# Kernel tuning notes

Measured on AMD Instinct MI355X. Metric: run time of the kernel, lower is better.

The kernel has to match this reference:

```python
import jax, jax.numpy as jnp
import numpy as np
from jax import lax

EPS = 1e-06


def setup_inputs() -> dict:
    key = jax.random.key(0)
    # mel-spectrogram energies: non-negative, shape (batch, n_mels, time)
    E = jax.random.uniform(key, (32, 256, 4096), dtype=jnp.float32)
    s = jnp.array([0.025], dtype=jnp.float32)
    alpha = jnp.array([0.98], dtype=jnp.float32)
    delta = jnp.array([2.0], dtype=jnp.float32)
    r = jnp.array([0.25], dtype=jnp.float32)
    return {"E": E, "s": s, "alpha": alpha, "delta": delta, "r": r}


def _iir(E, s):
    # first-order EMA over the last (time) axis: M[t] = (1-s)*M[t-1] + s*E[t], M[0] = E[0]
    s_c = jnp.clip(s, 0.0, 1.0)[0]  # scalar
    xT = jnp.moveaxis(E, -1, 0)  # (T, B, F) time-major for scan

    def step(m, x):
        m = (1.0 - s_c) * m + s_c * x
        return m, m

    _, MT = lax.scan(step, xT[0], xT[1:])
    M = jnp.concatenate([xT[:1], MT], axis=0)  # (T, B, F)
    return jnp.moveaxis(M, 0, -1)  # (B, F, T)


def reference(E, s, alpha, delta, r):
    # NOTE: original torch code computes clamped alpha/r but then uses the
    # raw self.alpha / self.r in the PCEN formula; we reproduce that exactly.
    M = _iir(E, s)
    pcen = (E / (EPS + M) ** alpha + delta) ** r - delta ** r
    pmin = pcen.min()
    pmax = pcen.max()
    return 2.0 * (pcen - pmin) / (pmax - pmin) - 1.0
```

## Files before the change

kernel.cpp:

```cpp
#include <hip/hip_runtime.h>

static constexpr int T_LEN = 4096;
static constexpr int GROUPS = T_LEN / 256;
#define EPSV 1e-6f

typedef float vfloat4 __attribute__((ext_vector_type(4)));

__device__ __forceinline__ float fexp2(float x) { return __builtin_amdgcn_exp2f(x); }
__device__ __forceinline__ float flog2(float x) { return __builtin_amdgcn_logf(x); }

__device__ __forceinline__ unsigned int flip_f(float f) {
    unsigned int u = __float_as_uint(f);
    return u ^ ((u >> 31) ? 0xFFFFFFFFu : 0x80000000u);
}
__device__ __forceinline__ float unflip_f(unsigned int u) {
    u ^= ((u >> 31) ? 0x80000000u : 0xFFFFFFFFu);
    return __uint_as_float(u);
}

__global__ void init_ws(unsigned int* ws) {
    ws[0] = 0xFFFFFFFFu;
    ws[1] = 0x00000000u;
}

template <int PASS>
__launch_bounds__(256, 4)
__global__ void pcen_pass(const float* __restrict__ E,
                          const float* __restrict__ sp,
                          const float* __restrict__ ap,
                          const float* __restrict__ dp,
                          const float* __restrict__ rp,
                          float* __restrict__ out,
                          unsigned int* __restrict__ ws,
                          int rows)
{
    const int tid  = threadIdx.x;
    const int lane = tid & 63;
    const int wv   = tid >> 6;
    const int row  = blockIdx.x * 4 + wv;

    float s = sp[0];
    s = fminf(fmaxf(s, 0.0f), 1.0f);
    const float a     = 1.0f - s;
    const float alpha = ap[0];
    const float delta = dp[0];
    const float r     = rp[0];
    const float na    = -alpha;
    const float dr    = fexp2(r * flog2(delta));

    const float a2 = a * a, a4 = a2 * a2, a8 = a4 * a4, a16 = a8 * a8,
                a32 = a16 * a16, a64 = a32 * a32, a128 = a64 * a64,
                a256 = a128 * a128;
    float pwl;
    if (a > 0.0f) pwl = fexp2((float)(4 * lane) * flog2(a));
    else          pwl = (lane == 0) ? 1.0f : 0.0f;

    float scale = 0.0f, bias = 0.0f;
    if (PASS == 1) {
        const float pmin = unflip_f(ws[0]);
        const float pmax = unflip_f(ws[1]);
        const float inv  = 2.0f / (pmax - pmin);
        scale = inv;
        bias  = __builtin_fmaf(-pmin, inv, -1.0f);
    }

    float vmin = __builtin_inff(), vmax = -__builtin_inff();

    if (row < rows) {
        const float4* __restrict__ src = (const float4*)(E + (size_t)row * T_LEN);
        float* __restrict__ drow = out + (size_t)row * T_LEN;

        float carry = E[(size_t)row * T_LEN];
        float4 cur = src[lane];

        for (int g = 0; g < GROUPS; ++g) {
            float4 nxt = make_float4(0.f, 0.f, 0.f, 0.f);
            if (g + 1 < GROUPS) nxt = src[(g + 1) * 64 + lane];

            float b = cur.x;
            b = __builtin_fmaf(a, b, cur.y);
            b = __builtin_fmaf(a, b, cur.z);
            b = __builtin_fmaf(a, b, cur.w);
            float B = s * b;

            float t;
            t = __shfl_up(B, 1, 64);  if (lane >= 1)  B = __builtin_fmaf(a4,   t, B);
            t = __shfl_up(B, 2, 64);  if (lane >= 2)  B = __builtin_fmaf(a8,   t, B);
            t = __shfl_up(B, 4, 64);  if (lane >= 4)  B = __builtin_fmaf(a16,  t, B);
            t = __shfl_up(B, 8, 64);  if (lane >= 8)  B = __builtin_fmaf(a32,  t, B);
            t = __shfl_up(B, 16, 64); if (lane >= 16) B = __builtin_fmaf(a64,  t, B);
            t = __shfl_up(B, 32, 64); if (lane >= 32) B = __builtin_fmaf(a128, t, B);

            float Bex = __shfl_up(B, 1, 64);
            if (lane == 0) Bex = 0.0f;
            const float B63 = __shfl(B, 63, 64);

            float m = __builtin_fmaf(pwl, carry, Bex);
            carry   = __builtin_fmaf(a256, carry, B63);

            float4 o;
            float p;
            m = __builtin_fmaf(a, m, s * cur.x);
            p = fexp2(r * flog2(__builtin_fmaf(cur.x, fexp2(na * flog2(EPSV + m)), delta))) - dr;
            if (PASS == 0) { vmin = fminf(vmin, p); vmax = fmaxf(vmax, p); }
            else            o.x = __builtin_fmaf(p, scale, bias);

            m = __builtin_fmaf(a, m, s * cur.y);
            p = fexp2(r * flog2(__builtin_fmaf(cur.y, fexp2(na * flog2(EPSV + m)), delta))) - dr;
            if (PASS == 0) { vmin = fminf(vmin, p); vmax = fmaxf(vmax, p); }
            else            o.y = __builtin_fmaf(p, scale, bias);

            m = __builtin_fmaf(a, m, s * cur.z);
            p = fexp2(r * flog2(__builtin_fmaf(cur.z, fexp2(na * flog2(EPSV + m)), delta))) - dr;
            if (PASS == 0) { vmin = fminf(vmin, p); vmax = fmaxf(vmax, p); }
            else            o.z = __builtin_fmaf(p, scale, bias);

            m = __builtin_fmaf(a, m, s * cur.w);
            p = fexp2(r * flog2(__builtin_fmaf(cur.w, fexp2(na * flog2(EPSV + m)), delta))) - dr;
            if (PASS == 0) { vmin = fminf(vmin, p); vmax = fmaxf(vmax, p); }
            else            o.w = __builtin_fmaf(p, scale, bias);

            if (PASS == 1) {
                vfloat4 ov = { o.x, o.y, o.z, o.w };
                __builtin_nontemporal_store(ov, (vfloat4*)(drow + (size_t)(g * 64 + lane) * 4));
            }
            cur = nxt;
        }
    }

    if (PASS == 0) {
        for (int off = 32; off >= 1; off >>= 1) {
            vmin = fminf(vmin, __shfl_xor(vmin, off, 64));
            vmax = fmaxf(vmax, __shfl_xor(vmax, off, 64));
        }
        __shared__ unsigned int smin, smax;
        if (tid == 0) { smin = 0xFFFFFFFFu; smax = 0u; }
        __syncthreads();
        if (lane == 0 && row < rows) {
            atomicMin(&smin, flip_f(vmin));
            atomicMax(&smax, flip_f(vmax));
        }
        __syncthreads();
        if (tid == 0) {
            atomicMin(&ws[0], smin);
            atomicMax(&ws[1], smax);
        }
    }
}

extern "C" void kernel_launch(void* const* d_in, const int* in_sizes, int n_in,
                              void* d_out, int out_size, void* d_ws, size_t ws_size,
                              hipStream_t stream) {
    const float* E     = (const float*)d_in[0];
    const float* s     = (const float*)d_in[1];
    const float* alpha = (const float*)d_in[2];
    const float* delta = (const float*)d_in[3];
    const float* r     = (const float*)d_in[4];
    float* out         = (float*)d_out;
    unsigned int* ws   = (unsigned int*)d_ws;

    const int rows   = in_sizes[0] / T_LEN;
    const int blocks = (rows + 3) / 4;

    hipLaunchKernelGGL(init_ws, dim3(1), dim3(1), 0, stream, ws);
    hipLaunchKernelGGL((pcen_pass<0>), dim3(blocks), dim3(256), 0, stream,
                       E, s, alpha, delta, r, out, ws, rows);
    hipLaunchKernelGGL((pcen_pass<1>), dim3(blocks), dim3(256), 0, stream,
                       E, s, alpha, delta, r, out, ws, rows);
}
```

Before: 299.5 us.

## Give each lane a contiguous time chunk and skip pow in min/max pass

Each lane now loads 64 contiguous samples of the row into registers. It reduces them to one chunk sum, and a single wave-wide scan with power a64 replaces the 16 per-group scans that carried state across groups. The first pass now tracks min/max of the pre-power value u and applies the monotonic pow(u, r) only to the block extremes, which removes two transcendentals per element in that pass. The constant delta^r subtraction is dropped because it cancels in the min/max normalization. In exchange, global loads and stores become lane-strided (256 B apart) rather than coalesced, and register pressure rises from holding 16 float4 per lane.

```diff
diff --git a/kernel.cpp b/kernel.cpp
--- a/kernel.cpp
+++ b/kernel.cpp
@@ -1,7 +1,7 @@
 #include <hip/hip_runtime.h>
 
-static constexpr int T_LEN = 4096;
-static constexpr int GROUPS = T_LEN / 256;
+static constexpr int T_LEN  = 4096;
+static constexpr int CHUNKS = T_LEN / (64 * 4);
 #define EPSV 1e-6f
 
 typedef float vfloat4 __attribute__((ext_vector_type(4)));
@@ -42,17 +42,15 @@
     float s = sp[0];
     s = fminf(fmaxf(s, 0.0f), 1.0f);
     const float a     = 1.0f - s;
-    const float alpha = ap[0];
+    const float na    = -ap[0];
     const float delta = dp[0];
     const float r     = rp[0];
-    const float na    = -alpha;
-    const float dr    = fexp2(r * flog2(delta));
 
-    const float a2 = a * a, a4 = a2 * a2, a8 = a4 * a4, a16 = a8 * a8,
-                a32 = a16 * a16, a64 = a32 * a32, a128 = a64 * a64,
-                a256 = a128 * a128;
+    const float a2 = a * a, a4 = a2 * a2, a8 = a4 * a4,
+                a16 = a8 * a8, a32 = a16 * a16, a64 = a32 * a32;
+
     float pwl;
-    if (a > 0.0f) pwl = fexp2((float)(4 * lane) * flog2(a));
+    if (a > 0.0f) pwl = fexp2((float)(64 * lane) * flog2(a));
     else          pwl = (lane == 0) ? 1.0f : 0.0f;
 
     float scale = 0.0f, bias = 0.0f;
@@ -67,64 +65,72 @@
     float vmin = __builtin_inff(), vmax = -__builtin_inff();
 
     if (row < rows) {
-        const float4* __restrict__ src = (const float4*)(E + (size_t)row * T_LEN);
-        float* __restrict__ drow = out + (size_t)row * T_LEN;
+        const float4* __restrict__ src =
+            (const float4*)(E + (size_t)row * T_LEN) + lane * CHUNKS;
 
-        float carry = E[(size_t)row * T_LEN];
-        float4 cur = src[lane];
+        float4 v[CHUNKS];
+#pragma unroll
+        for (int j = 0; j < CHUNKS; ++j) v[j] = src[j];
 
-        for (int g = 0; g < GROUPS; ++g) {
-            float4 nxt = make_float4(0.f, 0.f, 0.f, 0.f);
-            if (g + 1 < GROUPS) nxt = src[(g + 1) * 64 + lane];
+        float w0 = 0.0f, w1 = 0.0f, w2 = 0.0f, w3 = 0.0f;
+#pragma unroll
+        for (int j = 0; j < CHUNKS; ++j) {
+            w0 = __builtin_fmaf(a4, w0, v[j].x);
+            w1 = __builtin_fmaf(a4, w1, v[j].y);
+            w2 = __builtin_fmaf(a4, w2, v[j].z);
+            w3 = __builtin_fmaf(a4, w3, v[j].w);
+        }
+        float W = s * __builtin_fmaf(a, __builtin_fmaf(a, __builtin_fmaf(a, w0, w1), w2), w3);
 
-            float b = cur.x;
-            b = __builtin_fmaf(a, b, cur.y);
-            b = __builtin_fmaf(a, b, cur.z);
-            b = __builtin_fmaf(a, b, cur.w);
-            float B = s * b;
+        float S = W, t, q = a64;
+        t = __shfl_up(S, 1, 64);  if (lane >= 1)  S = __builtin_fmaf(q, t, S); q *= q;
+        t = __shfl_up(S, 2, 64);  if (lane >= 2)  S = __builtin_fmaf(q, t, S); q *= q;
+        t = __shfl_up(S, 4, 64);  if (lane >= 4)  S = __builtin_fmaf(q, t, S); q *= q;
+        t = __shfl_up(S, 8, 64);  if (lane >= 8)  S = __builtin_fmaf(q, t, S); q *= q;
+        t = __shfl_up(S, 16, 64); if (lane >= 16) S = __builtin_fmaf(q, t, S); q *= q;
+        t = __shfl_up(S, 32, 64); if (lane >= 32) S = __builtin_fmaf(q, t, S);
 
-            float t;
-            t = __shfl_up(B, 1, 64);  if (lane >= 1)  B = __builtin_fmaf(a4,   t, B);
-            t = __shfl_up(B, 2, 64);  if (lane >= 2)  B = __builtin_fmaf(a8,   t, B);
-            t = __shfl_up(B, 4, 64);  if (lane >= 4)  B = __builtin_fmaf(a16,  t, B);
-            t = __shfl_up(B, 8, 64);  if (lane >= 8)  B = __builtin_fmaf(a32,  t, B);
-            t = __shfl_up(B, 16, 64); if (lane >= 16) B = __builtin_fmaf(a64,  t, B);
-            t = __shfl_up(B, 32, 64); if (lane >= 32) B = __builtin_fmaf(a128, t, B);
+        float Sex = __shfl_up(S, 1, 64);
+        if (lane == 0) Sex = 0.0f;
+        const float e0 = __shfl(v[0].x, 0, 64);
 
-            float Bex = __shfl_up(B, 1, 64);
-            if (lane == 0) Bex = 0.0f;
-            const float B63 = __shfl(B, 63, 64);
+        float m = __builtin_fmaf(pwl, e0, Sex);
 
-            float m = __builtin_fmaf(pwl, carry, Bex);
-            carry   = __builtin_fmaf(a256, carry, B63);
+        float* __restrict__ drow = out + (size_t)row * T_LEN + lane * (CHUNKS * 4);
 
+#pragma unroll
+        for (int j = 0; j < CHUNKS; ++j) {
             float4 o;
-            float p;
-            m = __builtin_fmaf(a, m, s * cur.x);
-            p = fexp2(r * flog2(__builtin_fmaf(cur.x, fexp2(na * flog2(EPSV + m)), delta))) - dr;
-            if (PASS == 0) { vmin = fminf(vmin, p); vmax = fmaxf(vmax, p); }
-            else            o.x = __builtin_fmaf(p, scale, bias);
+            float x, u;
 
-            m = __builtin_fmaf(a, m, s * cur.y);
-            p = fexp2(r * flog2(__builtin_fmaf(cur.y, fexp2(na * flog2(EPSV + m)), delta))) - dr;
-            if (PASS == 0) { vmin = fminf(vmin, p); vmax = fmaxf(vmax, p); }
-            else            o.y = __builtin_fmaf(p, scale, bias);
+            x = v[j].x;
+            m = __builtin_fmaf(a, m, s * x);
+            u = __builtin_fmaf(x, fexp2(na * flog2(EPSV + m)), delta);
+            if (PASS == 0) { vmin = fminf(vmin, u); vmax = fmaxf(vmax, u); }
+            else            o.x = __builtin_fmaf(fexp2(r * flog2(u)), scale, bias);
 
-            m = __builtin_fmaf(a, m, s * cur.z);
-            p = fexp2(r * flog2(__builtin_fmaf(cur.z, fexp2(na * flog2(EPSV + m)), delta))) - dr;
-            if (PASS == 0) { vmin = fminf(vmin, p); vmax = fmaxf(vmax, p); }
-            else            o.z = __builtin_fmaf(p, scale, bias);
+            x = v[j].y;
+            m = __builtin_fmaf(a, m, s * x);
+            u = __builtin_fmaf(x, fexp2(na * flog2(EPSV + m)), delta);
+            if (PASS == 0) { vmin = fminf(vmin, u); vmax = fmaxf(vmax, u); }
+            else            o.y = __builtin_fmaf(fexp2(r * flog2(u)), scale, bias);
 
-            m = __builtin_fmaf(a, m, s * cur.w);
-            p = fexp2(r * flog2(__builtin_fmaf(cur.w, fexp2(na * flog2(EPSV + m)), delta))) - dr;
-            if (PASS == 0) { vmin = fminf(vmin, p); vmax = fmaxf(vmax, p); }
-            else            o.w = __builtin_fmaf(p, scale, bias);
+            x = v[j].z;
+            m = __builtin_fmaf(a, m, s * x);
+            u = __builtin_fmaf(x, fexp2(na * flog2(EPSV + m)), delta);
+            if (PASS == 0) { vmin = fminf(vmin, u); vmax = fmaxf(vmax, u); }
+            else            o.z = __builtin_fmaf(fexp2(r * flog2(u)), scale, bias);
+
+            x = v[j].w;
+            m = __builtin_fmaf(a, m, s * x);
+            u = __builtin_fmaf(x, fexp2(na * flog2(EPSV + m)), delta);
+            if (PASS == 0) { vmin = fminf(vmin, u); vmax = fmaxf(vmax, u); }
+            else            o.w = __builtin_fmaf(fexp2(r * flog2(u)), scale, bias);
 
             if (PASS == 1) {
                 vfloat4 ov = { o.x, o.y, o.z, o.w };
-                __builtin_nontemporal_store(ov, (vfloat4*)(drow + (size_t)(g * 64 + lane) * 4));
+                __builtin_nontemporal_store(ov, (vfloat4*)(drow + j * 4));
             }
-            cur = nxt;
         }
     }
 
@@ -142,8 +148,12 @@
         }
         __syncthreads();
         if (tid == 0) {
-            atomicMin(&ws[0], smin);
-            atomicMax(&ws[1], smax);
+            const float umin = unflip_f(smin);
+            const float umax = unflip_f(smax);
+            const float pl = fexp2(r * flog2(umin));
+            const float ph = fexp2(r * flog2(umax));
+            atomicMin(&ws[0], flip_f(fminf(pl, ph)));
+            atomicMax(&ws[1], flip_f(fmaxf(pl, ph)));
         }
     }
 }
```

After: 580.5 us. 1.94x slower.

## Store intermediate PCEN base to output and normalize in a separate elementwise pass

Applied to the files above, without the earlier changes.

The first pass now writes the pre-power value u = E*M^-alpha + delta to the output buffer and tracks its min/max. Because the power r is monotone for positive r, the global extrema of the final value are derived from the extrema of u. A lightweight second kernel then applies the power and the affine normalization in place, and the delta^r term cancels out of the normalization. This replaces recomputing the scan in a second pass with a read-modify-write of the output, roughly 128 MB written plus 128 MB read and written again. It relies on r being positive so that the power preserves ordering, which the original formula does not guarantee.

```diff
diff --git a/kernel.cpp b/kernel.cpp
--- a/kernel.cpp
+++ b/kernel.cpp
@@ -23,9 +23,8 @@
     ws[1] = 0x00000000u;
 }
 
-template <int PASS>
 __launch_bounds__(256, 4)
-__global__ void pcen_pass(const float* __restrict__ E,
+__global__ void pcen_scan(const float* __restrict__ E,
                           const float* __restrict__ sp,
                           const float* __restrict__ ap,
                           const float* __restrict__ dp,
@@ -46,7 +45,6 @@
     const float delta = dp[0];
     const float r     = rp[0];
     const float na    = -alpha;
-    const float dr    = fexp2(r * flog2(delta));
 
     const float a2 = a * a, a4 = a2 * a2, a8 = a4 * a4, a16 = a8 * a8,
                 a32 = a16 * a16, a64 = a32 * a32, a128 = a64 * a64,
@@ -54,15 +52,6 @@
     float pwl;
     if (a > 0.0f) pwl = fexp2((float)(4 * lane) * flog2(a));
     else          pwl = (lane == 0) ? 1.0f : 0.0f;
-
-    float scale = 0.0f, bias = 0.0f;
-    if (PASS == 1) {
-        const float pmin = unflip_f(ws[0]);
-        const float pmax = unflip_f(ws[1]);
-        const float inv  = 2.0f / (pmax - pmin);
-        scale = inv;
-        bias  = __builtin_fmaf(-pmin, inv, -1.0f);
-    }
 
     float vmin = __builtin_inff(), vmax = -__builtin_inff();
 
@@ -99,52 +88,86 @@
             carry   = __builtin_fmaf(a256, carry, B63);
 
             float4 o;
-            float p;
-            m = __builtin_fmaf(a, m, s * cur.x);
-            p = fexp2(r * flog2(__builtin_fmaf(cur.x, fexp2(na * flog2(EPSV + m)), delta))) - dr;
-            if (PASS == 0) { vmin = fminf(vmin, p); vmax = fmaxf(vmax, p); }
-            else            o.x = __builtin_fmaf(p, scale, bias);
+            float x, u;
 
-            m = __builtin_fmaf(a, m, s * cur.y);
-            p = fexp2(r * flog2(__builtin_fmaf(cur.y, fexp2(na * flog2(EPSV + m)), delta))) - dr;
-            if (PASS == 0) { vmin = fminf(vmin, p); vmax = fmaxf(vmax, p); }
-            else            o.y = __builtin_fmaf(p, scale, bias);
+            x = cur.x;
+            m = __builtin_fmaf(a, m, s * x);
+            u = __builtin_fmaf(x, fexp2(na * flog2(EPSV + m)), delta);
+            vmin = fminf(vmin, u); vmax = fmaxf(vmax, u);
+            o.x = u;
 
-            m = __builtin_fmaf(a, m, s * cur.z);
-            p = fexp2(r * flog2(__builtin_fmaf(cur.z, fexp2(na * flog2(EPSV + m)), delta))) - dr;
-            if (PASS == 0) { vmin = fminf(vmin, p); vmax = fmaxf(vmax, p); }
-            else            o.z = __builtin_fmaf(p, scale, bias);
+            x = cur.y;
+            m = __builtin_fmaf(a, m, s * x);
+            u = __builtin_fmaf(x, fexp2(na * flog2(EPSV + m)), delta);
+            vmin = fminf(vmin, u); vmax = fmaxf(vmax, u);
+            o.y = u;
 
-            m = __builtin_fmaf(a, m, s * cur.w);
-            p = fexp2(r * flog2(__builtin_fmaf(cur.w, fexp2(na * flog2(EPSV + m)), delta))) - dr;
-            if (PASS == 0) { vmin = fminf(vmin, p); vmax = fmaxf(vmax, p); }
-            else            o.w = __builtin_fmaf(p, scale, bias);
+            x = cur.z;
+            m = __builtin_fmaf(a, m, s * x);
+            u = __builtin_fmaf(x, fexp2(na * flog2(EPSV + m)), delta);
+            vmin = fminf(vmin, u); vmax = fmaxf(vmax, u);
+            o.z = u;
 
-            if (PASS == 1) {
-                vfloat4 ov = { o.x, o.y, o.z, o.w };
-                __builtin_nontemporal_store(ov, (vfloat4*)(drow + (size_t)(g * 64 + lane) * 4));
-            }
+            x = cur.w;
+            m = __builtin_fmaf(a, m, s * x);
+            u = __builtin_fmaf(x, fexp2(na * flog2(EPSV + m)), delta);
+            vmin = fminf(vmin, u); vmax = fmaxf(vmax, u);
+            o.w = u;
+
+            vfloat4 ov = { o.x, o.y, o.z, o.w };
+            *((vfloat4*)(drow + (size_t)(g * 64 + lane) * 4)) = ov;
+
             cur = nxt;
         }
     }
 
-    if (PASS == 0) {
-        for (int off = 32; off >= 1; off >>= 1) {
-            vmin = fminf(vmin, __shfl_xor(vmin, off, 64));
-            vmax = fmaxf(vmax, __shfl_xor(vmax, off, 64));
-        }
-        __shared__ unsigned int smin, smax;
-        if (tid == 0) { smin = 0xFFFFFFFFu; smax = 0u; }
-        __syncthreads();
-        if (lane == 0 && row < rows) {
-            atomicMin(&smin, flip_f(vmin));
-            atomicMax(&smax, flip_f(vmax));
-        }
-        __syncthreads();
-        if (tid == 0) {
-            atomicMin(&ws[0], smin);
-            atomicMax(&ws[1], smax);
-        }
+    for (int off = 32; off >= 1; off >>= 1) {
+        vmin = fminf(vmin, __shfl_xor(vmin, off, 64));
+        vmax = fmaxf(vmax, __shfl_xor(vmax, off, 64));
+    }
+    __shared__ unsigned int smin, smax;
+    if (tid == 0) { smin = 0xFFFFFFFFu; smax = 0u; }
+    __syncthreads();
+    if (lane == 0 && row < rows) {
+        atomicMin(&smin, flip_f(vmin));
+        atomicMax(&smax, flip_f(vmax));
+    }
+    __syncthreads();
+    if (tid == 0) {
+        const float umin = unflip_f(smin);
+        const float umax = unflip_f(smax);
+        const float pl = fexp2(r * flog2(umin));
+        const float ph = fexp2(r * flog2(umax));
+        atomicMin(&ws[0], flip_f(fminf(pl, ph)));
+        atomicMax(&ws[1], flip_f(fmaxf(pl, ph)));
+    }
+}
+
+__launch_bounds__(256, 8)
+__global__ void pcen_norm(float* __restrict__ out,
+                          const float* __restrict__ rp,
+                          const unsigned int* __restrict__ ws,
+                          int n4)
+{
+    const float r    = rp[0];
+    const float pmin = unflip_f(ws[0]);
+    const float pmax = unflip_f(ws[1]);
+    const float inv  = 2.0f / (pmax - pmin);
+    const float bias = __builtin_fmaf(-pmin, inv, -1.0f);
+
+    const vfloat4* __restrict__ ip = (const vfloat4*)out;
+    vfloat4* __restrict__ op = (vfloat4*)out;
+
+    int idx = blockIdx.x * 256 + threadIdx.x;
+    const int stride = gridDim.x * 256;
+    for (; idx < n4; idx += stride) {
+        vfloat4 u = ip[idx];
+        vfloat4 o;
+        o.x = __builtin_fmaf(fexp2(r * flog2(u.x)), inv, bias);
+        o.y = __builtin_fmaf(fexp2(r * flog2(u.y)), inv, bias);
+        o.z = __builtin_fmaf(fexp2(r * flog2(u.z)), inv, bias);
+        o.w = __builtin_fmaf(fexp2(r * flog2(u.w)), inv, bias);
+        __builtin_nontemporal_store(o, op + idx);
     }
 }
 
@@ -162,9 +185,12 @@
     const int rows   = in_sizes[0] / T_LEN;
     const int blocks = (rows + 3) / 4;
 
+    const int n4      = (rows * T_LEN) / 4;
+    const int blocks1 = 2048;
+
     hipLaunchKernelGGL(init_ws, dim3(1), dim3(1), 0, stream, ws);
-    hipLaunchKernelGGL((pcen_pass<0>), dim3(blocks), dim3(256), 0, stream,
+    hipLaunchKernelGGL(pcen_scan, dim3(blocks), dim3(256), 0, stream,
                        E, s, alpha, delta, r, out, ws, rows);
-    hipLaunchKernelGGL((pcen_pass<1>), dim3(blocks), dim3(256), 0, stream,
-                       E, s, alpha, delta, r, out, ws, rows);
+    hipLaunchKernelGGL(pcen_norm, dim3(blocks1), dim3(256), 0, stream,
+                       out, r, ws, n4);
 }
```

Measured after the change: 304.3 us. No clear change (+1.6%).
